# Kernel tuning notes

Measured on AMD Instinct MI355X. Metric: run time of the kernel, lower is better.

## Reference

```python
import jax, jax.numpy as jnp
import numpy as np

N = 30000   # nodes
E = 600000  # edges (avg degree 20)
H = 128     # hidden_channels
L = 4       # num_layers
G = 64      # graphs in batch


def _init(key, shape, fan_in):
    return (jax.random.normal(key, shape, jnp.float32) / np.sqrt(fan_in)).astype(jnp.float32)


def setup_inputs() -> dict:
    key = jax.random.key(0)
    ks = jax.random.split(key, 24)
    x = jax.random.normal(ks[0], (N, 1), jnp.float32)
    pos = jax.random.normal(ks[1], (N, 3), jnp.float32)
    edge_index = jax.random.randint(ks[2], (2, E), 0, N, dtype=jnp.int32).astype(jnp.int64)
    batch = jnp.sort(jax.random.randint(ks[3], (N,), 0, G, dtype=jnp.int32)).astype(jnp.int64)

    emb_w = _init(ks[4], (1, H), 1)
    emb_b = jnp.zeros((H,), jnp.float32)

    # stacked per-layer params: msg MLP (2H+1 -> H -> H), node MLP (2H -> H -> H)
    msg_w1 = _init(ks[5], (L, 2 * H + 1, H), 2 * H + 1)
    msg_b1 = jnp.zeros((L, H), jnp.float32)
    msg_w2 = _init(ks[6], (L, H, H), H)
    msg_b2 = jnp.zeros((L, H), jnp.float32)
    node_w1 = _init(ks[7], (L, 2 * H, H), 2 * H)
    node_b1 = jnp.zeros((L, H), jnp.float32)
    node_w2 = _init(ks[8], (L, H, H), H)
    node_b2 = jnp.zeros((L, H), jnp.float32)

    out_w1 = _init(ks[9], (H, 32), H)
    out_b1 = jnp.zeros((32,), jnp.float32)
    out_w2 = _init(ks[10], (32, 1), 32)
    out_b2 = jnp.zeros((1,), jnp.float32)

    return {
        "x": x, "pos": pos, "edge_index": edge_index, "batch": batch,
        "emb_w": emb_w, "emb_b": emb_b,
        "msg_w1": msg_w1, "msg_b1": msg_b1, "msg_w2": msg_w2, "msg_b2": msg_b2,
        "node_w1": node_w1, "node_b1": node_b1, "node_w2": node_w2, "node_b2": node_b2,
        "out_w1": out_w1, "out_b1": out_b1, "out_w2": out_w2, "out_b2": out_b2,
    }


def reference(x, pos, edge_index, batch,
              emb_w, emb_b,
              msg_w1, msg_b1, msg_w2, msg_b2,
              node_w1, node_b1, node_w2, node_b2,
              out_w1, out_b1, out_w2, out_b2):
    row, col = edge_index[0], edge_index[1]  # row = source j, col = target i
    # edge scalar: squared distance (computed once, reused across layers)
    dist_sq = jnp.sum((pos[row] - pos[col]) ** 2, axis=-1, keepdims=True)  # [E,1]

    h = x @ emb_w + emb_b  # [N,H]
    for l in range(L):
        x_j = h[row]   # source features
        x_i = h[col]   # target features
        m = jnp.concatenate([x_i, x_j, dist_sq], axis=-1)           # [E, 2H+1]
        m = jax.nn.silu(m @ msg_w1[l] + msg_b1[l]) @ msg_w2[l] + msg_b2[l]  # [E,H]
        aggr = jax.ops.segment_sum(m, col, num_segments=N)          # scatter-add to targets
        nh = jnp.concatenate([h, aggr], axis=-1)                    # [N, 2H]
        h = jax.nn.silu(nh @ node_w1[l] + node_b1[l]) @ node_w2[l] + node_b2[l]
        # dropout omitted for deterministic reference (eval mode)

    g = jax.ops.segment_sum(h, batch, num_segments=G)               # global_add_pool [G,H]
    return jax.nn.silu(g @ out_w1 + out_b1) @ out_w2 + out_b2       # [G,1]
```

## Files before the change

### kernel.cpp

```cpp
#include <hip/hip_runtime.h>

typedef unsigned short u16;
typedef __bf16 bf16x8 __attribute__((ext_vector_type(8)));
typedef float f32x4 __attribute__((ext_vector_type(4)));

#define HN 128
#define TM 64
#define ASTRIDE 136
#define ECH 256

__device__ __forceinline__ u16 f2bf(float f) {
  union { float f; unsigned u; } v; v.f = f;
  unsigned r = v.u + 0x7fffu + ((v.u >> 16) & 1u);
  return (u16)(r >> 16);
}
__device__ __forceinline__ float bf2f(u16 v) {
  union { unsigned u; float f; } x; x.u = ((unsigned)v) << 16; return x.f;
}
__device__ __forceinline__ float bflo(unsigned v) {
  union { unsigned u; float f; } x; x.u = v << 16; return x.f;
}
__device__ __forceinline__ float bfhi(unsigned v) {
  union { unsigned u; float f; } x; x.u = v & 0xffff0000u; return x.f;
}
__device__ __forceinline__ float silu_f(float x) {
  float e = __builtin_amdgcn_exp2f(-1.442695041f * x);
  return x * __builtin_amdgcn_rcpf(1.f + e);
}

__global__ void pack_weights(const float* __restrict__ msg_w1, const float* __restrict__ msg_w2,
                             const float* __restrict__ node_w1, const float* __restrict__ node_w2,
                             u16* __restrict__ pw, int* __restrict__ deg,
                             float* __restrict__ g, int N_, int GH) {
  int id = blockIdx.x * 256 + threadIdx.x;
  if (id < N_) deg[id] = 0;
  if (id < GH) g[id] = 0.f;
  if (id >= 4 * 6 * 16384) return;
  int l = id / (6 * 16384);
  int rem = id % (6 * 16384);
  int m = rem / 16384;
  int e = rem % 16384;
  int kg = e >> 10;
  int n = (e >> 3) & 127;
  int j = e & 7;
  int k = kg * 8 + j;
  float v = 0.f;
  switch (m) {
    case 0: v = msg_w1[(l * 257 + k) * 128 + n]; break;
    case 1: v = msg_w1[(l * 257 + 128 + k) * 128 + n]; break;
    case 2: v = msg_w2[(l * 128 + k) * 128 + n]; break;
    case 3: v = node_w1[(l * 256 + k) * 128 + n]; break;
    case 4: v = node_w1[(l * 256 + 128 + k) * 128 + n]; break;
    case 5: v = node_w2[(l * 128 + k) * 128 + n]; break;
  }
  pw[id] = f2bf(v);
}

__device__ __forceinline__ void gemm64(const u16* s_A, const u16* s_W,
                                       int w, int quad, int m16, f32x4 acc[8]) {
#pragma unroll
  for (int ks = 0; ks < 4; ks++) {
    bf16x8 a = *(const bf16x8*)&s_A[(w * 16 + m16) * ASTRIDE + ks * 32 + quad * 8];
#pragma unroll
    for (int ct = 0; ct < 8; ct++) {
      bf16x8 b = *(const bf16x8*)&s_W[(ks * 4 + quad) * 1024 + (ct * 16 + m16) * 8];
      acc[ct] = __builtin_amdgcn_mfma_f32_16x16x32_bf16(a, b, acc[ct], 0, 0, 0);
    }
  }
}

__global__ __launch_bounds__(256) void fold_kernel(
    const float* __restrict__ msg_w2, const float* __restrict__ node_w1,
    const float* __restrict__ msg_b2, const u16* __restrict__ pw,
    u16* __restrict__ pwc, float* __restrict__ vc) {
  __shared__ __align__(16) u16 s_A[TM * ASTRIDE];
  __shared__ __align__(16) u16 s_W[16384];
  const int t = threadIdx.x;
  const int w = t >> 6, lane = t & 63, quad = lane >> 4, m16 = lane & 15;
  const int b = blockIdx.x, l = b >> 1, half = b & 1;
  const int tile0 = half * 64;

  {
    int r = t >> 2, qo = (t & 3) * 32;
    const float4* src = (const float4*)(msg_w2 + (size_t)(l * 128 + tile0 + r) * 128 + qo);
    u16* dst = s_A + r * ASTRIDE + qo;
#pragma unroll
    for (int i = 0; i < 8; i++) {
      float4 v = src[i];
      ushort4 o;
      o.x = f2bf(v.x); o.y = f2bf(v.y); o.z = f2bf(v.z); o.w = f2bf(v.w);
      *(ushort4*)(dst + i * 4) = o;
    }
  }
  {
    const int4* src = (const int4*)(pw + (size_t)(l * 6 + 4) * 16384);
    int4* dst = (int4*)s_W;
#pragma unroll
    for (int i = 0; i < 8; i++) dst[t + i * 256] = src[t + i * 256];
  }
  __syncthreads();
  f32x4 acc[8];
#pragma unroll
  for (int ct = 0; ct < 8; ct++) acc[ct] = {0.f, 0.f, 0.f, 0.f};
  gemm64(s_A, s_W, w, quad, m16, acc);
#pragma unroll
  for (int ct = 0; ct < 8; ct++)
#pragma unroll
    for (int j = 0; j < 4; j++) {
      int k = tile0 + w * 16 + quad * 4 + j;
      int n = ct * 16 + m16;
      pwc[(size_t)l * 16384 + (k >> 3) * 1024 + n * 8 + (k & 7)] = f2bf(acc[ct][j]);
    }
  if (half == 0 && t < 128) {
    float s = 0.f;
    for (int np = 0; np < 128; np++)
      s += msg_b2[l * 128 + np] * node_w1[(size_t)(l * 256 + 128 + np) * 128 + t];
    vc[l * 128 + t] = s;
  }
}

__global__ void hist_kernel(const int* __restrict__ eidx, int* __restrict__ deg,
                            int* __restrict__ rnk, int E_) {
  int e = blockIdx.x * 256 + threadIdx.x;
  if (e < E_) rnk[e] = atomicAdd(&deg[eidx[E_ + e]], 1);
}

__global__ void scan1_kernel(const int* __restrict__ deg, int* __restrict__ off,
                             int* __restrict__ bsum, int n) {
  __shared__ int s[256];
  int t = threadIdx.x;
  int i = blockIdx.x * 256 + t;
  int v = (i < n) ? deg[i] : 0;
  s[t] = v;
  for (int d = 1; d < 256; d <<= 1) {
    __syncthreads();
    int x = (t >= d) ? s[t - d] : 0;
    __syncthreads();
    s[t] += x;
  }
  __syncthreads();
  if (i < n) off[i] = s[t] - v;
  if (t == 255) bsum[blockIdx.x] = s[255];
}

__global__ void scan2_kernel(int* __restrict__ bsum, int nb) {
  __shared__ int s[256];
  int t = threadIdx.x;
  int v = (t < nb) ? bsum[t] : 0;
  s[t] = v;
  for (int d = 1; d < 256; d <<= 1) {
    __syncthreads();
    int x = (t >= d) ? s[t - d] : 0;
    __syncthreads();
    s[t] += x;
  }
  __syncthreads();
  if (t < nb) bsum[t] = s[t] - v;
}

__global__ void scan3_kernel(int* __restrict__ off, const int* __restrict__ bsum, int n) {
  int i = blockIdx.x * 256 + threadIdx.x;
  if (i < n) off[i] += bsum[blockIdx.x];
}

__global__ void scatter_kernel(const int* __restrict__ eidx, const float* __restrict__ pos,
                               const int* __restrict__ off, const int* __restrict__ rnk,
                               int4* __restrict__ es16, int E_) {
  int e = blockIdx.x * 256 + threadIdx.x;
  if (e >= E_) return;
  int sr = eidx[e], tg = eidx[E_ + e];
  float dx = pos[sr * 3 + 0] - pos[tg * 3 + 0];
  float dy = pos[sr * 3 + 1] - pos[tg * 3 + 1];
  float dz = pos[sr * 3 + 2] - pos[tg * 3 + 2];
  float d = dx * dx + dy * dy + dz * dz;
  int p = off[tg] + rnk[e];
  int4 v;
  v.x = sr; v.y = tg; v.z = __float_as_int(d); v.w = 0;
  es16[p] = v;
}

__global__ __launch_bounds__(256) void proj_kernel(
    const float* __restrict__ x, const float* __restrict__ emb_w,
    const float* __restrict__ emb_b, u16* __restrict__ hbf,
    u16* __restrict__ Pout, u16* __restrict__ Qout,
    const u16* __restrict__ pw, const float* __restrict__ b1,
    float* __restrict__ S, int NHtot, int nblocks, int nnodes) {
  __shared__ __align__(16) u16 s_A[TM * ASTRIDE];
  __shared__ __align__(16) u16 s_W[16384];
  const int t = threadIdx.x;
  const int w = t >> 6, lane = t & 63, quad = lane >> 4, m16 = lane & 15;
  const int tile0 = blockIdx.x * TM;
  {
    int id = blockIdx.x * 256 + t;
    int stride = nblocks * 256;
    for (int i = id; i < NHtot; i += stride) S[i] = 0.f;
  }
  {
    int r = t >> 2, qo = (t & 3) * 32;
    int node = tile0 + r;
    if (node >= nnodes) node = nnodes - 1;
    float xv = x[node];
    u16 hv[32];
#pragma unroll
    for (int i = 0; i < 32; i++) hv[i] = f2bf(xv * emb_w[qo + i] + emb_b[qo + i]);
    u16* dst = s_A + r * ASTRIDE + qo;
#pragma unroll
    for (int i = 0; i < 4; i++) *(int4*)(dst + i * 8) = *(int4*)(hv + i * 8);
    u16* gd = hbf + (size_t)node * HN + qo;
#pragma unroll
    for (int i = 0; i < 4; i++) *(int4*)(gd + i * 8) = *(int4*)(hv + i * 8);
  }
  {
    const int4* src = (const int4*)pw;
    int4* dst = (int4*)s_W;
#pragma unroll
    for (int i = 0; i < 8; i++) dst[t + i * 256] = src[t + i * 256];
  }
  __syncthreads();
  f32x4 acc[8];
#pragma unroll
  for (int ct = 0; ct < 8; ct++) acc[ct] = {0.f, 0.f, 0.f, 0.f};
  gemm64(s_A, s_W, w, quad, m16, acc);
  __syncthreads();
  {
    const int4* src = (const int4*)(pw + 16384);
    int4* dst = (int4*)s_W;
#pragma unroll
    for (int i = 0; i < 8; i++) dst[t + i * 256] = src[t + i * 256];
  }
  float bb[8];
#pragma unroll
  for (int ct = 0; ct < 8; ct++) bb[ct] = b1[ct * 16 + m16];
#pragma unroll
  for (int ct = 0; ct < 8; ct++)
#pragma unroll
    for (int j = 0; j < 4; j++) {
      int n = tile0 + w * 16 + quad * 4 + j;
      if (n < nnodes) Pout[n * HN + ct * 16 + m16] = f2bf(acc[ct][j] + bb[ct]);
    }
  __syncthreads();
#pragma unroll
  for (int ct = 0; ct < 8; ct++) acc[ct] = {0.f, 0.f, 0.f, 0.f};
  gemm64(s_A, s_W, w, quad, m16, acc);
#pragma unroll
  for (int ct = 0; ct < 8; ct++)
#pragma unroll
    for (int j = 0; j < 4; j++) {
      int n = tile0 + w * 16 + quad * 4 + j;
      if (n < nnodes) Qout[n * HN + ct * 16 + m16] = f2bf(acc[ct][j]);
    }
}

__device__ __forceinline__ void edge_step(
    int tg_s, float dd_s, unsigned qv,
    int& cur_s, float& p0, float& p1, float& s0, float& s1,
    const u16* __restrict__ P, float* __restrict__ S, int cp,
    float wd0, float wd1, int tprev_s, int tnext_s) {
  if (tg_s != cur_s) {
    if (cur_s >= 0) {
      float* dst = &S[(size_t)cur_s * HN + cp];
      if (cur_s == tprev_s || cur_s == tnext_s) {
        atomicAdd(dst, s0);
        atomicAdd(dst + 1, s1);
      } else {
        float2 v = {s0, s1};
        *(float2*)dst = v;
      }
    }
    cur_s = tg_s; s0 = 0.f; s1 = 0.f;
    int cg = tg_s < 0 ? 0 : tg_s;
    unsigned pv = *(const unsigned*)&P[(size_t)cg * HN + cp];
    p0 = bflo(pv); p1 = bfhi(pv);
  }
  float x0 = p0 + bflo(qv) + dd_s * wd0;
  float x1 = p1 + bfhi(qv) + dd_s * wd1;
  s0 += silu_f(x0);
  s1 += silu_f(x1);
}

__global__ __launch_bounds__(256) void edge_kernel(
    const u16* __restrict__ P, const u16* __restrict__ Q,
    float* __restrict__ S, const float* __restrict__ w1d,
    const int4* __restrict__ es16, int E_) {
  __shared__ int s_src[ECH + 8];
  __shared__ int s_tgt[ECH + 8];
  __shared__ float s_dist[ECH + 8];

  const int t = threadIdx.x;
  const int e0 = blockIdx.x * ECH;
  {
    int e = e0 + t;
    if (e < E_) {
      int4 v = es16[e];
      s_src[t] = v.x;
      s_tgt[t] = v.y;
      s_dist[t] = __int_as_float(v.z);
    } else {
      s_src[t] = 0; s_tgt[t] = -1; s_dist[t] = 0.f;
    }
    if (t < 8) { s_src[ECH + t] = 0; s_tgt[ECH + t] = -1; s_dist[ECH + t] = 0.f; }
  }
  __syncthreads();

  const int lane = t & 63;
  const int w = t >> 6;
  const int cp = lane * 2;
  const int a = w * 64;
  const float2 wdv = *(const float2*)&w1d[cp];
  const float wd0 = wdv.x, wd1 = wdv.y;

  int tprev_s, tnext_s;
  if (w == 0) tprev_s = (e0 > 0) ? es16[e0 - 1].y : -2;
  else tprev_s = s_tgt[a - 1];
  if (w == 3) tnext_s = (e0 + ECH < E_) ? es16[e0 + ECH].y : -2;
  else tnext_s = s_tgt[a + 64];
  tprev_s = __builtin_amdgcn_readfirstlane(tprev_s);
  tnext_s = __builtin_amdgcn_readfirstlane(tnext_s);

  int tg[8];
  float dd[8];
  unsigned qv[8];
#pragma unroll
  for (int j = 0; j < 8; j++) {
    tg[j] = s_tgt[a + j];
    dd[j] = s_dist[a + j];
    qv[j] = *(const unsigned*)&Q[(size_t)s_src[a + j] * HN + cp];
  }

  int cur_s = -1;
  float s0 = 0.f, s1 = 0.f, p0 = 0.f, p1 = 0.f;

#pragma unroll
  for (int i = a; i < a + 64; i += 8) {
    int tgn[8];
    float ddn[8];
    unsigned qvn[8];
#pragma unroll
    for (int j = 0; j < 8; j++) {
      int idx = i + 8 + j;
      tgn[j] = s_tgt[idx];
      ddn[j] = s_dist[idx];
      qvn[j] = *(const unsigned*)&Q[(size_t)s_src[idx] * HN + cp];
    }
#pragma unroll
    for (int j = 0; j < 8; j++) {
      int tg_s = __builtin_amdgcn_readfirstlane(tg[j]);
      edge_step(tg_s, dd[j], qv[j], cur_s, p0, p1, s0, s1, P, S, cp, wd0, wd1, tprev_s, tnext_s);
    }
#pragma unroll
    for (int j = 0; j < 8; j++) { tg[j] = tgn[j]; dd[j] = ddn[j]; qv[j] = qvn[j]; }
  }

  if (cur_s >= 0) {
    float* dst = &S[(size_t)cur_s * HN + cp];
    if (cur_s == tprev_s || cur_s == tnext_s) {
      atomicAdd(dst, s0);
      atomicAdd(dst + 1, s1);
    } else {
      float2 v = {s0, s1};
      *(float2*)dst = v;
    }
  }
}

template <bool FUSE>
__global__ __launch_bounds__(256) void node_kernel(
    const u16* __restrict__ hbf, float* __restrict__ S, const int* __restrict__ deg,
    u16* __restrict__ hout, const u16* __restrict__ pwc, const float* __restrict__ vc,
    const u16* __restrict__ pwn, const float* __restrict__ b1, const float* __restrict__ b2,
    const u16* __restrict__ pw_next, const float* __restrict__ b1_next,
    u16* __restrict__ Pout, u16* __restrict__ Qout, int nnodes) {
  __shared__ __align__(16) u16 s_A[TM * ASTRIDE];
  __shared__ __align__(16) u16 s_W[16384];
  const int t = threadIdx.x;
  const int w = t >> 6, lane = t & 63, quad = lane >> 4, m16 = lane & 15;
  const int tile0 = blockIdx.x * TM;
  const int r_ = t >> 2, qo_ = (t & 3) * 32;
  int node_ = tile0 + r_;
  if (node_ >= nnodes) node_ = nnodes - 1;

  {
    const int4* src = (const int4*)pwc;
    int4* dst = (int4*)s_W;
#pragma unroll
    for (int i = 0; i < 8; i++) dst[t + i * 256] = src[t + i * 256];
  }
  {
    const float4* src = (const float4*)(S + (size_t)node_ * HN + qo_);
    u16* dst = s_A + r_ * ASTRIDE + qo_;
#pragma unroll
    for (int i = 0; i < 8; i++) {
      float4 v = src[i];
      ushort4 o;
      o.x = f2bf(v.x); o.y = f2bf(v.y); o.z = f2bf(v.z); o.w = f2bf(v.w);
      *(ushort4*)(dst + i * 4) = o;
    }
    float4 z = {0.f, 0.f, 0.f, 0.f};
    float4* zd = (float4*)(S + (size_t)node_ * HN + qo_);
#pragma unroll
    for (int i = 0; i < 8; i++) zd[i] = z;
  }
  __syncthreads();

  f32x4 acc[8];
#pragma unroll
  for (int ct = 0; ct < 8; ct++) acc[ct] = {0.f, 0.f, 0.f, 0.f};
  gemm64(s_A, s_W, w, quad, m16, acc);
  __syncthreads();

  {
    const int4* src = (const int4*)pwn;
    int4* dst = (int4*)s_W;
#pragma unroll
    for (int i = 0; i < 8; i++) dst[t + i * 256] = src[t + i * 256];
  }
  {
    const int4* src = (const int4*)(hbf + (size_t)node_ * HN + qo_);
    int4* dst = (int4*)(s_A + r_ * ASTRIDE + qo_);
#pragma unroll
    for (int i = 0; i < 4; i++) dst[i] = src[i];
  }
  __syncthreads();
  gemm64(s_A, s_W, w, quad, m16, acc);
  __syncthreads();

  {
    const int4* src = (const int4*)(pwn + 32768);
    int4* dst = (int4*)s_W;
#pragma unroll
    for (int i = 0; i < 8; i++) dst[t + i * 256] = src[t + i * 256];
  }
  {
    float bb1[8], vcr[8];
#pragma unroll
    for (int ct = 0; ct < 8; ct++) {
      bb1[ct] = b1[ct * 16 + m16];
      vcr[ct] = vc[ct * 16 + m16];
    }
    float degv[4];
#pragma unroll
    for (int j = 0; j < 4; j++) {
      int n = tile0 + w * 16 + quad * 4 + j;
      if (n >= nnodes) n = nnodes - 1;
      degv[j] = (float)deg[n];
    }
#pragma unroll
    for (int ct = 0; ct < 8; ct++)
#pragma unroll
      for (int j = 0; j < 4; j++) {
        int row = w * 16 + quad * 4 + j;
        float xv = acc[ct][j] + bb1[ct] + degv[j] * vcr[ct];
        s_A[row * ASTRIDE + ct * 16 + m16] = f2bf(silu_f(xv));
      }
  }
  __syncthreads();

#pragma unroll
  for (int ct = 0; ct < 8; ct++) acc[ct] = {0.f, 0.f, 0.f, 0.f};
  gemm64(s_A, s_W, w, quad, m16, acc);

  float bb2[8];
#pragma unroll
  for (int ct = 0; ct < 8; ct++) bb2[ct] = b2[ct * 16 + m16];
#pragma unroll
  for (int ct = 0; ct < 8; ct++)
#pragma unroll
    for (int j = 0; j < 4; j++) {
      int row = w * 16 + quad * 4 + j;
      int n = tile0 + row;
      if (n < nnodes) hout[n * HN + ct * 16 + m16] = f2bf(acc[ct][j] + bb2[ct]);
    }

  if (FUSE) {
#pragma unroll
    for (int ct = 0; ct < 8; ct++)
#pragma unroll
      for (int j = 0; j < 4; j++) {
        int row = w * 16 + quad * 4 + j;
        s_A[row * ASTRIDE + ct * 16 + m16] = f2bf(acc[ct][j] + bb2[ct]);
      }
    __syncthreads();
    {
      const int4* src = (const int4*)pw_next;
      int4* dst = (int4*)s_W;
#pragma unroll
      for (int i = 0; i < 8; i++) dst[t + i * 256] = src[t + i * 256];
    }
    __syncthreads();
#pragma unroll
    for (int ct = 0; ct < 8; ct++) acc[ct] = {0.f, 0.f, 0.f, 0.f};
    gemm64(s_A, s_W, w, quad, m16, acc);
    {
      float bbn[8];
#pragma unroll
      for (int ct = 0; ct < 8; ct++) bbn[ct] = b1_next[ct * 16 + m16];
#pragma unroll
      for (int ct = 0; ct < 8; ct++)
#pragma unroll
        for (int j = 0; j < 4; j++) {
          int n = tile0 + w * 16 + quad * 4 + j;
          if (n < nnodes) Pout[n * HN + ct * 16 + m16] = f2bf(acc[ct][j] + bbn[ct]);
        }
    }
    __syncthreads();
    {
      const int4* src = (const int4*)(pw_next + 16384);
      int4* dst = (int4*)s_W;
#pragma unroll
      for (int i = 0; i < 8; i++) dst[t + i * 256] = src[t + i * 256];
    }
    __syncthreads();
#pragma unroll
    for (int ct = 0; ct < 8; ct++) acc[ct] = {0.f, 0.f, 0.f, 0.f};
    gemm64(s_A, s_W, w, quad, m16, acc);
#pragma unroll
    for (int ct = 0; ct < 8; ct++)
#pragma unroll
      for (int j = 0; j < 4; j++) {
        int n = tile0 + w * 16 + quad * 4 + j;
        if (n < nnodes) Qout[n * HN + ct * 16 + m16] = f2bf(acc[ct][j]);
      }
  }
}

__global__ __launch_bounds__(256) void pool_kernel(
    const u16* __restrict__ h, const int* __restrict__ batch,
    float* __restrict__ g, int N) {
  __shared__ int s_b[64];
  const int t = threadIdx.x;
  const int n0 = blockIdx.x * 64;
  if (t < 64) {
    int n = n0 + t;
    s_b[t] = (n < N) ? batch[n] : -1;
  }
  __syncthreads();
  const int cp = (t & 63) * 2;
  const int rg = t >> 6;
  int cur = -1;
  float s0 = 0.f, s1 = 0.f;
#pragma unroll 4
  for (int i = 0; i < 16; i++) {
    int r = rg * 16 + i;
    int b = s_b[r];
    if (b < 0) break;
    if (b != cur) {
      if (cur >= 0) {
        atomicAdd(&g[cur * HN + cp], s0);
        atomicAdd(&g[cur * HN + cp + 1], s1);
      }
      cur = b; s0 = 0.f; s1 = 0.f;
    }
    unsigned v = *(const unsigned*)&h[(size_t)(n0 + r) * HN + cp];
    s0 += bf2f((u16)(v & 0xffffu));
    s1 += bf2f((u16)(v >> 16));
  }
  if (cur >= 0) {
    atomicAdd(&g[cur * HN + cp], s0);
    atomicAdd(&g[cur * HN + cp + 1], s1);
  }
}

__global__ __launch_bounds__(64) void out_kernel(
    const float* __restrict__ g, const float* __restrict__ w1,
    const float* __restrict__ b1, const float* __restrict__ w2,
    const float* __restrict__ b2, float* __restrict__ out) {
  const int gi = blockIdx.x;
  const int t = threadIdx.x;
  const int c = t & 31, kh = t >> 5;
  float s = 0.f;
  for (int k = kh * 64; k < kh * 64 + 64; k++)
    s += g[gi * HN + k] * w1[k * 32 + c];
  s += __shfl_down(s, 32);
  float r = 0.f;
  if (kh == 0) r = silu_f(s + b1[c]) * w2[c];
  r += __shfl_down(r, 16);
  r += __shfl_down(r, 8);
  r += __shfl_down(r, 4);
  r += __shfl_down(r, 2);
  r += __shfl_down(r, 1);
  if (t == 0) out[gi] = r + b2[0];
}

extern "C" void kernel_launch(void* const* d_in, const int* in_sizes, int n_in,
                              void* d_out, int out_size, void* d_ws, size_t ws_size,
                              hipStream_t stream) {
  const float* x = (const float*)d_in[0];
  const float* pos = (const float*)d_in[1];
  const int* eidx = (const int*)d_in[2];
  const int* batch = (const int*)d_in[3];
  const float* emb_w = (const float*)d_in[4];
  const float* emb_b = (const float*)d_in[5];
  const float* msg_w1 = (const float*)d_in[6];
  const float* msg_b1 = (const float*)d_in[7];
  const float* msg_w2 = (const float*)d_in[8];
  const float* msg_b2 = (const float*)d_in[9];
  const float* node_w1 = (const float*)d_in[10];
  const float* node_b1 = (const float*)d_in[11];
  const float* node_w2 = (const float*)d_in[12];
  const float* node_b2 = (const float*)d_in[13];
  const float* out_w1 = (const float*)d_in[14];
  const float* out_b1 = (const float*)d_in[15];
  const float* out_w2 = (const float*)d_in[16];
  const float* out_b2 = (const float*)d_in[17];
  float* outp = (float*)d_out;

  const int N = 30000, E = 600000, G = 64;
  const size_t NH = (size_t)N * HN;

  u16* hA = (u16*)d_ws;
  u16* hB = hA + NH;
  u16* Pp = hB + NH;
  u16* Qp = Pp + NH;
  float* S = (float*)(Qp + NH);
  int4* es16 = (int4*)(S + NH);
  int* deg = (int*)(es16 + E);
  int* off = deg + N;
  int* bsum = off + N;
  float* g = (float*)(bsum + 128);
  u16* pw = (u16*)(g + G * HN);
  u16* pwc = pw + (size_t)4 * 6 * 16384;
  float* vcb = (float*)(pwc + (size_t)4 * 16384);
  int* rnk = (int*)S;

  const int NB = (N + 255) / 256;
  const int NTB = (N + TM - 1) / TM;

  pack_weights<<<(4 * 6 * 16384 + 255) / 256, 256, 0, stream>>>(
      msg_w1, msg_w2, node_w1, node_w2, pw, deg, g, N, G * HN);
  fold_kernel<<<8, 256, 0, stream>>>(msg_w2, node_w1, msg_b2, pw, pwc, vcb);

  hist_kernel<<<(E + 255) / 256, 256, 0, stream>>>(eidx, deg, rnk, E);
  scan1_kernel<<<NB, 256, 0, stream>>>(deg, off, bsum, N);
  scan2_kernel<<<1, 256, 0, stream>>>(bsum, NB);
  scan3_kernel<<<NB, 256, 0, stream>>>(off, bsum, N);
  scatter_kernel<<<(E + 255) / 256, 256, 0, stream>>>(eidx, pos, off, rnk, es16, E);

  proj_kernel<<<NTB, 256, 0, stream>>>(x, emb_w, emb_b, hA, Pp, Qp, pw, msg_b1,
                                       S, (int)NH, NTB, N);

  u16* hcur = hA;
  u16* hnext = hB;
  for (int l = 0; l < 4; l++) {
    const u16* pwl = pw + (size_t)(l * 6) * 16384;
    edge_kernel<<<(E + ECH - 1) / ECH, 256, 0, stream>>>(
        Pp, Qp, S,
        msg_w1 + (size_t)(l * 257 + 256) * 128,
        es16, E);
    if (l < 3) {
      const u16* pw_next = pw + (size_t)((l + 1) * 6) * 16384;
      node_kernel<true><<<NTB, 256, 0, stream>>>(
          hcur, S, deg, hnext, pwc + (size_t)l * 16384, vcb + l * 128,
          pwl + 3 * 16384, node_b1 + l * 128, node_b2 + l * 128,
          pw_next, msg_b1 + (l + 1) * 128, Pp, Qp, N);
    } else {
      node_kernel<false><<<NTB, 256, 0, stream>>>(
          hcur, S, deg, hnext, pwc + (size_t)l * 16384, vcb + l * 128,
          pwl + 3 * 16384, node_b1 + l * 128, node_b2 + l * 128,
          nullptr, nullptr, nullptr, nullptr, N);
    }
    u16* tmp = hcur; hcur = hnext; hnext = tmp;
  }

  pool_kernel<<<(N + 63) / 64, 256, 0, stream>>>(hcur, batch, g, N);
  out_kernel<<<G, 64, 0, stream>>>(g, out_w1, out_b1, out_w2, out_b2, outp);
}
```

Before: 401.7 us.

## Compact edge records to 8 bytes and prefetch weight tiles into registers

Edge records now pack source and target into one 32-bit word (15-bit source, target in the upper bits) next to the float distance. This halves the per-edge record traffic that each edge kernel launch reads. In proj_kernel and node_kernel, the next weight tile and the h rows are loaded from global memory into registers before each GEMM, then written to shared memory after the barrier, so global latency overlaps with MFMA work. The S zeroing is also vectorised to float4; the costs are higher register pressure and a packing scheme that only holds while node count fits in 15 bits and target<<15 stays within int range.

```diff
diff --git a/kernel.cpp b/kernel.cpp
--- a/kernel.cpp
+++ b/kernel.cpp
@@ -165,7 +165,7 @@
 
 __global__ void scatter_kernel(const int* __restrict__ eidx, const float* __restrict__ pos,
                                const int* __restrict__ off, const int* __restrict__ rnk,
-                               int4* __restrict__ es16, int E_) {
+                               int2* __restrict__ es8, int E_) {
   int e = blockIdx.x * 256 + threadIdx.x;
   if (e >= E_) return;
   int sr = eidx[e], tg = eidx[E_ + e];
@@ -174,9 +174,10 @@
   float dz = pos[sr * 3 + 2] - pos[tg * 3 + 2];
   float d = dx * dx + dy * dy + dz * dz;
   int p = off[tg] + rnk[e];
-  int4 v;
-  v.x = sr; v.y = tg; v.z = __float_as_int(d); v.w = 0;
-  es16[p] = v;
+  int2 v;
+  v.x = sr | (tg << 15);
+  v.y = __float_as_int(d);
+  es8[p] = v;
 }
 
 __global__ __launch_bounds__(256) void proj_kernel(
@@ -184,16 +185,26 @@
     const float* __restrict__ emb_b, u16* __restrict__ hbf,
     u16* __restrict__ Pout, u16* __restrict__ Qout,
     const u16* __restrict__ pw, const float* __restrict__ b1,
-    float* __restrict__ S, int NHtot, int nblocks, int nnodes) {
+    float* __restrict__ S, int NH4, int nblocks, int nnodes) {
   __shared__ __align__(16) u16 s_A[TM * ASTRIDE];
   __shared__ __align__(16) u16 s_W[16384];
   const int t = threadIdx.x;
   const int w = t >> 6, lane = t & 63, quad = lane >> 4, m16 = lane & 15;
   const int tile0 = blockIdx.x * TM;
-  {
+
+  int4 wq[8];
+  {
+    const int4* src = (const int4*)pw;
+#pragma unroll
+    for (int i = 0; i < 8; i++) wq[i] = src[t + i * 256];
+  }
+  __builtin_amdgcn_sched_barrier(0);
+  {
+    float4* S4 = (float4*)S;
     int id = blockIdx.x * 256 + t;
     int stride = nblocks * 256;
-    for (int i = id; i < NHtot; i += stride) S[i] = 0.f;
+    float4 z = {0.f, 0.f, 0.f, 0.f};
+    for (int i = id; i < NH4; i += stride) S4[i] = z;
   }
   {
     int r = t >> 2, qo = (t & 3) * 32;
@@ -211,22 +222,26 @@
     for (int i = 0; i < 4; i++) *(int4*)(gd + i * 8) = *(int4*)(hv + i * 8);
   }
   {
-    const int4* src = (const int4*)pw;
     int4* dst = (int4*)s_W;
 #pragma unroll
-    for (int i = 0; i < 8; i++) dst[t + i * 256] = src[t + i * 256];
-  }
-  __syncthreads();
+    for (int i = 0; i < 8; i++) dst[t + i * 256] = wq[i];
+  }
+  __syncthreads();
+  {
+    const int4* src = (const int4*)(pw + 16384);
+#pragma unroll
+    for (int i = 0; i < 8; i++) wq[i] = src[t + i * 256];
+  }
+  __builtin_amdgcn_sched_barrier(0);
   f32x4 acc[8];
 #pragma unroll
   for (int ct = 0; ct < 8; ct++) acc[ct] = {0.f, 0.f, 0.f, 0.f};
   gemm64(s_A, s_W, w, quad, m16, acc);
   __syncthreads();
   {
-    const int4* src = (const int4*)(pw + 16384);
     int4* dst = (int4*)s_W;
 #pragma unroll
-    for (int i = 0; i < 8; i++) dst[t + i * 256] = src[t + i * 256];
+    for (int i = 0; i < 8; i++) dst[t + i * 256] = wq[i];
   }
   float bb[8];
 #pragma unroll
@@ -281,7 +296,7 @@
 __global__ __launch_bounds__(256) void edge_kernel(
     const u16* __restrict__ P, const u16* __restrict__ Q,
     float* __restrict__ S, const float* __restrict__ w1d,
-    const int4* __restrict__ es16, int E_) {
+    const int2* __restrict__ es8, int E_) {
   __shared__ int s_src[ECH + 8];
   __shared__ int s_tgt[ECH + 8];
   __shared__ float s_dist[ECH + 8];
@@ -291,10 +306,10 @@
   {
     int e = e0 + t;
     if (e < E_) {
-      int4 v = es16[e];
-      s_src[t] = v.x;
-      s_tgt[t] = v.y;
-      s_dist[t] = __int_as_float(v.z);
+      int2 v = es8[e];
+      s_src[t] = v.x & 0x7fff;
+      s_tgt[t] = v.x >> 15;
+      s_dist[t] = __int_as_float(v.y);
     } else {
       s_src[t] = 0; s_tgt[t] = -1; s_dist[t] = 0.f;
     }
@@ -310,9 +325,9 @@
   const float wd0 = wdv.x, wd1 = wdv.y;
 
   int tprev_s, tnext_s;
-  if (w == 0) tprev_s = (e0 > 0) ? es16[e0 - 1].y : -2;
+  if (w == 0) tprev_s = (e0 > 0) ? (es8[e0 - 1].x >> 15) : -2;
   else tprev_s = s_tgt[a - 1];
-  if (w == 3) tnext_s = (e0 + ECH < E_) ? es16[e0 + ECH].y : -2;
+  if (w == 3) tnext_s = (e0 + ECH < E_) ? (es8[e0 + ECH].x >> 15) : -2;
   else tnext_s = s_tgt[a + 64];
   tprev_s = __builtin_amdgcn_readfirstlane(tprev_s);
   tnext_s = __builtin_amdgcn_readfirstlane(tnext_s);
@@ -379,12 +394,13 @@
   int node_ = tile0 + r_;
   if (node_ >= nnodes) node_ = nnodes - 1;
 
+  int4 wq[8];
   {
     const int4* src = (const int4*)pwc;
-    int4* dst = (int4*)s_W;
-#pragma unroll
-    for (int i = 0; i < 8; i++) dst[t + i * 256] = src[t + i * 256];
-  }
+#pragma unroll
+    for (int i = 0; i < 8; i++) wq[i] = src[t + i * 256];
+  }
+  __builtin_amdgcn_sched_barrier(0);
   {
     const float4* src = (const float4*)(S + (size_t)node_ * HN + qo_);
     u16* dst = s_A + r_ * ASTRIDE + qo_;
@@ -400,35 +416,56 @@
 #pragma unroll
     for (int i = 0; i < 8; i++) zd[i] = z;
   }
-  __syncthreads();
-
+  {
+    int4* dst = (int4*)s_W;
+#pragma unroll
+    for (int i = 0; i < 8; i++) dst[t + i * 256] = wq[i];
+  }
+  __syncthreads();
+
+  int4 ha[4];
+  {
+    const int4* srca = (const int4*)(hbf + (size_t)node_ * HN + qo_);
+#pragma unroll
+    for (int i = 0; i < 4; i++) ha[i] = srca[i];
+    const int4* srcw = (const int4*)pwn;
+#pragma unroll
+    for (int i = 0; i < 8; i++) wq[i] = srcw[t + i * 256];
+  }
+  __builtin_amdgcn_sched_barrier(0);
   f32x4 acc[8];
 #pragma unroll
   for (int ct = 0; ct < 8; ct++) acc[ct] = {0.f, 0.f, 0.f, 0.f};
   gemm64(s_A, s_W, w, quad, m16, acc);
   __syncthreads();
-
-  {
-    const int4* src = (const int4*)pwn;
-    int4* dst = (int4*)s_W;
-#pragma unroll
-    for (int i = 0; i < 8; i++) dst[t + i * 256] = src[t + i * 256];
-  }
-  {
-    const int4* src = (const int4*)(hbf + (size_t)node_ * HN + qo_);
-    int4* dst = (int4*)(s_A + r_ * ASTRIDE + qo_);
-#pragma unroll
-    for (int i = 0; i < 4; i++) dst[i] = src[i];
-  }
-  __syncthreads();
+  {
+    int4* dsta = (int4*)(s_A + r_ * ASTRIDE + qo_);
+#pragma unroll
+    for (int i = 0; i < 4; i++) dsta[i] = ha[i];
+    int4* dstw = (int4*)s_W;
+#pragma unroll
+    for (int i = 0; i < 8; i++) dstw[t + i * 256] = wq[i];
+  }
+  __syncthreads();
+
+  {
+    const int4* srcw = (const int4*)(pwn + 32768);
+#pragma unroll
+    for (int i = 0; i < 8; i++) wq[i] = srcw[t + i * 256];
+  }
+  __builtin_amdgcn_sched_barrier(0);
   gemm64(s_A, s_W, w, quad, m16, acc);
   __syncthreads();
-
-  {
-    const int4* src = (const int4*)(pwn + 32768);
-    int4* dst = (int4*)s_W;
-#pragma unroll
-    for (int i = 0; i < 8; i++) dst[t + i * 256] = src[t + i * 256];
+  {
+    int4* dstw = (int4*)s_W;
+#pragma unroll
+    for (int i = 0; i < 8; i++) dstw[t + i * 256] = wq[i];
+  }
+  if (FUSE) {
+    const int4* srcw = (const int4*)pw_next;
+#pragma unroll
+    for (int i = 0; i < 8; i++) wq[i] = srcw[t + i * 256];
+    __builtin_amdgcn_sched_barrier(0);
   }
   {
     float bb1[8], vcr[8];
@@ -472,6 +509,12 @@
     }
 
   if (FUSE) {
+    __syncthreads();
+    {
+      int4* dstw = (int4*)s_W;
+#pragma unroll
+      for (int i = 0; i < 8; i++) dstw[t + i * 256] = wq[i];
+    }
 #pragma unroll
     for (int ct = 0; ct < 8; ct++)
 #pragma unroll
@@ -479,13 +522,12 @@
         int row = w * 16 + quad * 4 + j;
         s_A[row * ASTRIDE + ct * 16 + m16] = f2bf(acc[ct][j] + bb2[ct]);
       }
-    __syncthreads();
     {
-      const int4* src = (const int4*)pw_next;
-      int4* dst = (int4*)s_W;
-#pragma unroll
-      for (int i = 0; i < 8; i++) dst[t + i * 256] = src[t + i * 256];
-    }
+      const int4* srcw = (const int4*)(pw_next + 16384);
+#pragma unroll
+      for (int i = 0; i < 8; i++) wq[i] = srcw[t + i * 256];
+    }
+    __builtin_amdgcn_sched_barrier(0);
     __syncthreads();
 #pragma unroll
     for (int ct = 0; ct < 8; ct++) acc[ct] = {0.f, 0.f, 0.f, 0.f};
@@ -504,10 +546,9 @@
     }
     __syncthreads();
     {
-      const int4* src = (const int4*)(pw_next + 16384);
-      int4* dst = (int4*)s_W;
-#pragma unroll
-      for (int i = 0; i < 8; i++) dst[t + i * 256] = src[t + i * 256];
+      int4* dstw = (int4*)s_W;
+#pragma unroll
+      for (int i = 0; i < 8; i++) dstw[t + i * 256] = wq[i];
     }
     __syncthreads();
 #pragma unroll
@@ -612,8 +653,8 @@
   u16* Pp = hB + NH;
   u16* Qp = Pp + NH;
   float* S = (float*)(Qp + NH);
-  int4* es16 = (int4*)(S + NH);
-  int* deg = (int*)(es16 + E);
+  int2* es8 = (int2*)(S + NH);
+  int* deg = (int*)(es8 + E);
   int* off = deg + N;
   int* bsum = off + N;
   float* g = (float*)(bsum + 128);
@@ -633,10 +674,10 @@
   scan1_kernel<<<NB, 256, 0, stream>>>(deg, off, bsum, N);
   scan2_kernel<<<1, 256, 0, stream>>>(bsum, NB);
   scan3_kernel<<<NB, 256, 0, stream>>>(off, bsum, N);
-  scatter_kernel<<<(E + 255) / 256, 256, 0, stream>>>(eidx, pos, off, rnk, es16, E);
+  scatter_kernel<<<(E + 255) / 256, 256, 0, stream>>>(eidx, pos, off, rnk, es8, E);
 
   proj_kernel<<<NTB, 256, 0, stream>>>(x, emb_w, emb_b, hA, Pp, Qp, pw, msg_b1,
-                                       S, (int)NH, NTB, N);
+                                       S, (int)(NH / 4), NTB, N);
 
   u16* hcur = hA;
   u16* hnext = hB;
@@ -645,7 +686,7 @@
     edge_kernel<<<(E + ECH - 1) / ECH, 256, 0, stream>>>(
         Pp, Qp, S,
         msg_w1 + (size_t)(l * 257 + 256) * 128,
-        es16, E);
+        es8, E);
     if (l < 3) {
       const u16* pw_next = pw + (size_t)((l + 1) * 6) * 16384;
       node_kernel<true><<<NTB, 256, 0, stream>>>(
```

After: 468.7 us. 1.17x slower.

## Stage GEMM outputs through LDS for coalesced stores and pack edge records to 8 bytes

Applied to the files above, without the earlier changes.

GEMM epilogues in the projection and node kernels now write bf16 results into an LDS band (padded or XOR-swizzled) and then each lane stores full 16-byte rows to global memory. Before, the writes were scattered 2-byte stores. The sorted edge records shrink from 16 to 8 bytes by packing source and target into one 32-bit word with 15 and 17 bits. This cuts edge-list traffic in every layer. The S buffer is also zeroed with float4 stores. The packing relies on node indices below 32768, which holds for N=30000. The extra barriers and LDS reuse add some ordering risk.

```diff
diff --git a/kernel.cpp b/kernel.cpp
--- a/kernel.cpp
+++ b/kernel.cpp
@@ -26,6 +26,61 @@
 __device__ __forceinline__ float silu_f(float x) {
   float e = __builtin_amdgcn_exp2f(-1.442695041f * x);
   return x * __builtin_amdgcn_rcpf(1.f + e);
+}
+
+__device__ __forceinline__ void stage_store_sa(
+    u16* s_A, int w, int quad, int m16, int lane,
+    const f32x4 acc[8], const float bb[8],
+    u16* __restrict__ gdst, int tile0, int nnodes) {
+  u16* band = s_A + (w * 16) * ASTRIDE;
+#pragma unroll
+  for (int ct = 0; ct < 8; ct++)
+#pragma unroll
+    for (int j = 0; j < 4; j++) {
+      int row = quad * 4 + j;
+      band[row * ASTRIDE + ct * 16 + m16] = f2bf(acc[ct][j] + bb[ct]);
+    }
+  asm volatile("s_waitcnt lgkmcnt(0)" ::: "memory");
+  int row = lane >> 2, chunk = lane & 3;
+  int n = tile0 + w * 16 + row;
+  if (n < nnodes) {
+    const u16* rb = band + row * ASTRIDE + chunk * 32;
+    int4 v0 = *(const int4*)(rb + 0);
+    int4 v1 = *(const int4*)(rb + 8);
+    int4 v2 = *(const int4*)(rb + 16);
+    int4 v3 = *(const int4*)(rb + 24);
+    int4* gp = (int4*)(gdst + (size_t)n * HN + chunk * 32);
+    gp[0] = v0; gp[1] = v1; gp[2] = v2; gp[3] = v3;
+  }
+}
+
+__device__ __forceinline__ void stage_store_sw(
+    u16* s_W, int w, int quad, int m16, int lane,
+    const f32x4 acc[8], const float bb[8],
+    u16* __restrict__ gdst, int tile0, int nnodes) {
+  u16* band = s_W + w * 2048;
+#pragma unroll
+  for (int ct = 0; ct < 8; ct++)
+#pragma unroll
+    for (int j = 0; j < 4; j++) {
+      int row = quad * 4 + j;
+      int off = (row * 128 + ct * 16 + m16) ^ ((row & 7) << 3);
+      band[off] = f2bf(acc[ct][j] + bb[ct]);
+    }
+  asm volatile("s_waitcnt lgkmcnt(0)" ::: "memory");
+  int row = lane >> 2, chunk = lane & 3;
+  int n = tile0 + w * 16 + row;
+  if (n < nnodes) {
+    int4 v[4];
+#pragma unroll
+    for (int i = 0; i < 4; i++) {
+      int off = (row * 128 + chunk * 32 + i * 8) ^ ((row & 7) << 3);
+      v[i] = *(const int4*)(band + off);
+    }
+    int4* gp = (int4*)(gdst + (size_t)n * HN + chunk * 32);
+#pragma unroll
+    for (int i = 0; i < 4; i++) gp[i] = v[i];
+  }
 }
 
 __global__ void pack_weights(const float* __restrict__ msg_w1, const float* __restrict__ msg_w2,
@@ -165,7 +220,7 @@
 
 __global__ void scatter_kernel(const int* __restrict__ eidx, const float* __restrict__ pos,
                                const int* __restrict__ off, const int* __restrict__ rnk,
-                               int4* __restrict__ es16, int E_) {
+                               int2* __restrict__ es8, int E_) {
   int e = blockIdx.x * 256 + threadIdx.x;
   if (e >= E_) return;
   int sr = eidx[e], tg = eidx[E_ + e];
@@ -174,9 +229,10 @@
   float dz = pos[sr * 3 + 2] - pos[tg * 3 + 2];
   float d = dx * dx + dy * dy + dz * dz;
   int p = off[tg] + rnk[e];
-  int4 v;
-  v.x = sr; v.y = tg; v.z = __float_as_int(d); v.w = 0;
-  es16[p] = v;
+  int2 v;
+  v.x = sr | (tg << 15);
+  v.y = __float_as_int(d);
+  es8[p] = v;
 }
 
 __global__ __launch_bounds__(256) void proj_kernel(
@@ -184,16 +240,18 @@
     const float* __restrict__ emb_b, u16* __restrict__ hbf,
     u16* __restrict__ Pout, u16* __restrict__ Qout,
     const u16* __restrict__ pw, const float* __restrict__ b1,
-    float* __restrict__ S, int NHtot, int nblocks, int nnodes) {
+    float* __restrict__ S, int NH4, int nblocks, int nnodes) {
   __shared__ __align__(16) u16 s_A[TM * ASTRIDE];
   __shared__ __align__(16) u16 s_W[16384];
   const int t = threadIdx.x;
   const int w = t >> 6, lane = t & 63, quad = lane >> 4, m16 = lane & 15;
   const int tile0 = blockIdx.x * TM;
   {
+    float4* S4 = (float4*)S;
     int id = blockIdx.x * 256 + t;
     int stride = nblocks * 256;
-    for (int i = id; i < NHtot; i += stride) S[i] = 0.f;
+    float4 z = {0.f, 0.f, 0.f, 0.f};
+    for (int i = id; i < NH4; i += stride) S4[i] = z;
   }
   {
     int r = t >> 2, qo = (t & 3) * 32;
@@ -223,32 +281,26 @@
   gemm64(s_A, s_W, w, quad, m16, acc);
   __syncthreads();
   {
+    float bb[8];
+#pragma unroll
+    for (int ct = 0; ct < 8; ct++) bb[ct] = b1[ct * 16 + m16];
+    stage_store_sw(s_W, w, quad, m16, lane, acc, bb, Pout, tile0, nnodes);
+  }
+  __syncthreads();
+  {
     const int4* src = (const int4*)(pw + 16384);
     int4* dst = (int4*)s_W;
 #pragma unroll
     for (int i = 0; i < 8; i++) dst[t + i * 256] = src[t + i * 256];
   }
-  float bb[8];
-#pragma unroll
-  for (int ct = 0; ct < 8; ct++) bb[ct] = b1[ct * 16 + m16];
-#pragma unroll
-  for (int ct = 0; ct < 8; ct++)
-#pragma unroll
-    for (int j = 0; j < 4; j++) {
-      int n = tile0 + w * 16 + quad * 4 + j;
-      if (n < nnodes) Pout[n * HN + ct * 16 + m16] = f2bf(acc[ct][j] + bb[ct]);
-    }
   __syncthreads();
 #pragma unroll
   for (int ct = 0; ct < 8; ct++) acc[ct] = {0.f, 0.f, 0.f, 0.f};
   gemm64(s_A, s_W, w, quad, m16, acc);
-#pragma unroll
-  for (int ct = 0; ct < 8; ct++)
-#pragma unroll
-    for (int j = 0; j < 4; j++) {
-      int n = tile0 + w * 16 + quad * 4 + j;
-      if (n < nnodes) Qout[n * HN + ct * 16 + m16] = f2bf(acc[ct][j]);
-    }
+  {
+    float zz[8] = {0.f, 0.f, 0.f, 0.f, 0.f, 0.f, 0.f, 0.f};
+    stage_store_sa(s_A, w, quad, m16, lane, acc, zz, Qout, tile0, nnodes);
+  }
 }
 
 __device__ __forceinline__ void edge_step(
@@ -281,7 +333,7 @@
 __global__ __launch_bounds__(256) void edge_kernel(
     const u16* __restrict__ P, const u16* __restrict__ Q,
     float* __restrict__ S, const float* __restrict__ w1d,
-    const int4* __restrict__ es16, int E_) {
+    const int2* __restrict__ es8, int E_) {
   __shared__ int s_src[ECH + 8];
   __shared__ int s_tgt[ECH + 8];
   __shared__ float s_dist[ECH + 8];
@@ -291,10 +343,10 @@
   {
     int e = e0 + t;
     if (e < E_) {
-      int4 v = es16[e];
-      s_src[t] = v.x;
-      s_tgt[t] = v.y;
-      s_dist[t] = __int_as_float(v.z);
+      int2 v = es8[e];
+      s_src[t] = v.x & 0x7fff;
+      s_tgt[t] = v.x >> 15;
+      s_dist[t] = __int_as_float(v.y);
     } else {
       s_src[t] = 0; s_tgt[t] = -1; s_dist[t] = 0.f;
     }
@@ -310,9 +362,9 @@
   const float wd0 = wdv.x, wd1 = wdv.y;
 
   int tprev_s, tnext_s;
-  if (w == 0) tprev_s = (e0 > 0) ? es16[e0 - 1].y : -2;
+  if (w == 0) tprev_s = (e0 > 0) ? (es8[e0 - 1].x >> 15) : -2;
   else tprev_s = s_tgt[a - 1];
-  if (w == 3) tnext_s = (e0 + ECH < E_) ? es16[e0 + ECH].y : -2;
+  if (w == 3) tnext_s = (e0 + ECH < E_) ? (es8[e0 + ECH].x >> 15) : -2;
   else tnext_s = s_tgt[a + 64];
   tprev_s = __builtin_amdgcn_readfirstlane(tprev_s);
   tnext_s = __builtin_amdgcn_readfirstlane(tnext_s);
@@ -462,23 +514,10 @@
   float bb2[8];
 #pragma unroll
   for (int ct = 0; ct < 8; ct++) bb2[ct] = b2[ct * 16 + m16];
-#pragma unroll
-  for (int ct = 0; ct < 8; ct++)
-#pragma unroll
-    for (int j = 0; j < 4; j++) {
-      int row = w * 16 + quad * 4 + j;
-      int n = tile0 + row;
-      if (n < nnodes) hout[n * HN + ct * 16 + m16] = f2bf(acc[ct][j] + bb2[ct]);
-    }
+
+  stage_store_sa(s_A, w, quad, m16, lane, acc, bb2, hout, tile0, nnodes);
 
   if (FUSE) {
-#pragma unroll
-    for (int ct = 0; ct < 8; ct++)
-#pragma unroll
-      for (int j = 0; j < 4; j++) {
-        int row = w * 16 + quad * 4 + j;
-        s_A[row * ASTRIDE + ct * 16 + m16] = f2bf(acc[ct][j] + bb2[ct]);
-      }
     __syncthreads();
     {
       const int4* src = (const int4*)pw_next;
@@ -490,17 +529,12 @@
 #pragma unroll
     for (int ct = 0; ct < 8; ct++) acc[ct] = {0.f, 0.f, 0.f, 0.f};
     gemm64(s_A, s_W, w, quad, m16, acc);
+    __syncthreads();
     {
       float bbn[8];
 #pragma unroll
       for (int ct = 0; ct < 8; ct++) bbn[ct] = b1_next[ct * 16 + m16];
-#pragma unroll
-      for (int ct = 0; ct < 8; ct++)
-#pragma unroll
-        for (int j = 0; j < 4; j++) {
-          int n = tile0 + w * 16 + quad * 4 + j;
-          if (n < nnodes) Pout[n * HN + ct * 16 + m16] = f2bf(acc[ct][j] + bbn[ct]);
-        }
+      stage_store_sw(s_W, w, quad, m16, lane, acc, bbn, Pout, tile0, nnodes);
     }
     __syncthreads();
     {
@@ -513,13 +547,10 @@
 #pragma unroll
     for (int ct = 0; ct < 8; ct++) acc[ct] = {0.f, 0.f, 0.f, 0.f};
     gemm64(s_A, s_W, w, quad, m16, acc);
-#pragma unroll
-    for (int ct = 0; ct < 8; ct++)
-#pragma unroll
-      for (int j = 0; j < 4; j++) {
-        int n = tile0 + w * 16 + quad * 4 + j;
-        if (n < nnodes) Qout[n * HN + ct * 16 + m16] = f2bf(acc[ct][j]);
-      }
+    {
+      float zz[8] = {0.f, 0.f, 0.f, 0.f, 0.f, 0.f, 0.f, 0.f};
+      stage_store_sa(s_A, w, quad, m16, lane, acc, zz, Qout, tile0, nnodes);
+    }
   }
 }
 
@@ -612,8 +643,8 @@
   u16* Pp = hB + NH;
   u16* Qp = Pp + NH;
   float* S = (float*)(Qp + NH);
-  int4* es16 = (int4*)(S + NH);
-  int* deg = (int*)(es16 + E);
+  int2* es8 = (int2*)(S + NH);
+  int* deg = (int*)(es8 + E);
   int* off = deg + N;
   int* bsum = off + N;
   float* g = (float*)(bsum + 128);
@@ -633,10 +664,10 @@
   scan1_kernel<<<NB, 256, 0, stream>>>(deg, off, bsum, N);
   scan2_kernel<<<1, 256, 0, stream>>>(bsum, NB);
   scan3_kernel<<<NB, 256, 0, stream>>>(off, bsum, N);
-  scatter_kernel<<<(E + 255) / 256, 256, 0, stream>>>(eidx, pos, off, rnk, es16, E);
+  scatter_kernel<<<(E + 255) / 256, 256, 0, stream>>>(eidx, pos, off, rnk, es8, E);
 
   proj_kernel<<<NTB, 256, 0, stream>>>(x, emb_w, emb_b, hA, Pp, Qp, pw, msg_b1,
-                                       S, (int)NH, NTB, N);
+                                       S, (int)(NH / 4), NTB, N);
 
   u16* hcur = hA;
   u16* hnext = hB;
@@ -645,7 +676,7 @@
     edge_kernel<<<(E + ECH - 1) / ECH, 256, 0, stream>>>(
         Pp, Qp, S,
         msg_w1 + (size_t)(l * 257 + 256) * 128,
-        es16, E);
+        es8, E);
     if (l < 3) {
       const u16* pw_next = pw + (size_t)((l + 1) * 6) * 16384;
       node_kernel<true><<<NTB, 256, 0, stream>>>(
```

After: 405.5 us. About the same (+0.9%).
